# Kernel optimization log

Measured on AMD Instinct MI355X. Metric: run time of the kernel, lower is better.

## Reference

```python
import jax, jax.numpy as jnp
import numpy as np

N = 100000   # nodes
E = 1600000  # edges
IN = 92      # input node feature dim
H = 128      # hidden dim
B = 512      # graphs in batch
GI = 107     # global_info feature dim
L = 5        # conv layers
EPS = 1e-5   # batchnorm eps


def setup_inputs() -> dict:
    key = jax.random.key(0)
    ks = jax.random.split(key, 32)
    s = 0.05
    rn = lambda k, shp: jax.random.normal(k, shp, jnp.float32) * s
    return {
        "x": jax.random.normal(ks[0], (N, IN), jnp.float32),
        "edge_index": jax.random.randint(ks[1], (2, E), 0, N, jnp.int32),
        "edge_dist": jax.random.uniform(ks[2], (E,), jnp.float32),
        "global_info": jax.random.normal(ks[3], (N, GI), jnp.float32),
        "batch": jnp.sort(jax.random.randint(ks[4], (N,), 0, B, jnp.int32)),
        # input projection
        "lin_W": rn(ks[5], (IN, H)), "lin_b": rn(ks[6], (H,)),
        # GCN conv stack
        "conv_W": rn(ks[7], (L, H, H)), "conv_b": rn(ks[8], (L, H)),
        # shared batchnorm affine
        "bn_g": jnp.ones((H,), jnp.float32), "bn_b": jnp.zeros((H,), jnp.float32),
        # global attention
        "gat_in_W": rn(ks[9], (H + GI, H)), "gat_in_b": rn(ks[10], (H,)),
        "gat_lin_W": rn(ks[11], (2, H, H)), "gat_lin_b": rn(ks[12], (2, H)),
        "gat_out_W": rn(ks[13], (H, 1)), "gat_out_b": rn(ks[14], (1,)),
        # Set2Set LSTM (input 2H, hidden H)
        "lstm_Wih": rn(ks[15], (4 * H, 2 * H)), "lstm_Whh": rn(ks[16], (4 * H, H)),
        "lstm_bih": rn(ks[17], (4 * H,)), "lstm_bhh": rn(ks[18], (4 * H,)),
        # MLP head (in_dim = 2H)
        "mlp_W": rn(ks[19], (2 * H, 2 * H)), "mlp_b": rn(ks[20], (2 * H,)),
        "out1_W": rn(ks[21], (2 * H, 32)), "out1_b": rn(ks[22], (32,)),
        "out2_W": rn(ks[23], (32, 1)), "out2_b": rn(ks[24], (1,)),
    }


def _segment_softmax(e, seg, num_seg):
    m = jax.ops.segment_max(e, seg, num_seg)
    ex = jnp.exp(e - m[seg])
    return ex / jax.ops.segment_sum(ex, seg, num_seg)[seg]


def reference(x, edge_index, edge_dist, global_info, batch,
              lin_W, lin_b, conv_W, conv_b, bn_g, bn_b,
              gat_in_W, gat_in_b, gat_lin_W, gat_lin_b, gat_out_W, gat_out_b,
              lstm_Wih, lstm_Whh, lstm_bih, lstm_bhh,
              mlp_W, mlp_b, out1_W, out1_b, out2_W, out2_b):
    src, dst = edge_index[0], edge_index[1]

    x = jax.nn.relu(x @ lin_W + lin_b)

    # GCN normalization (improved=True: self-loop weight 2), identical each layer
    deg = jax.ops.segment_sum(edge_dist, dst, N) + 2.0
    dinv = jax.lax.rsqrt(deg)
    enorm = dinv[src] * edge_dist * dinv[dst]   # [E]
    self_norm = 2.0 * dinv * dinv               # [N]

    prev = x
    for l in range(L):
        xw = x @ conv_W[l]                                                  # [N,H]
        agg = (jax.ops.segment_sum(enorm[:, None] * xw[src], dst, N)
               + self_norm[:, None] * xw + conv_b[l])
        mu = agg.mean(0)
        var = agg.var(0)
        h = bn_g * (agg - mu) * jax.lax.rsqrt(var + EPS) + bn_b             # BN (batch stats)
        x = h + prev                                                         # residual; dropout=identity (eval)
        prev = x

    # global attention -> per-graph softmax node weights
    g = jax.nn.relu(jnp.concatenate([x, global_info], axis=-1) @ gat_in_W + gat_in_b)
    for l in range(2):
        g = jax.nn.relu(g @ gat_lin_W[l] + gat_lin_b[l])
    e = (g @ gat_out_W + gat_out_b)[:, 0]                                    # [N]
    w = _segment_softmax(e, batch, B)
    x = x * w[:, None]

    # Set2Set pooling, 3 processing steps
    hs = jnp.zeros((B, H), x.dtype)
    cs = jnp.zeros((B, H), x.dtype)
    q_star = jnp.zeros((B, 2 * H), x.dtype)
    for _ in range(3):
        gates = q_star @ lstm_Wih.T + hs @ lstm_Whh.T + lstm_bih + lstm_bhh
        i, f, gg, o = jnp.split(gates, 4, axis=-1)
        cs = jax.nn.sigmoid(f) * cs + jax.nn.sigmoid(i) * jnp.tanh(gg)
        hs = jax.nn.sigmoid(o) * jnp.tanh(cs)
        q = hs                                                                # [B,H]
        en = jnp.sum(x * q[batch], axis=-1)                                   # [N]
        a = _segment_softmax(en, batch, B)
        r = jax.ops.segment_sum(a[:, None] * x, batch, B)                      # [B,H]
        q_star = jnp.concatenate([q, r], axis=-1)

    # MLP head
    y = jax.nn.relu(q_star @ mlp_W + mlp_b)
    y = jax.nn.relu(y @ out1_W + out1_b)
    y = y @ out2_W + out2_b
    return y.reshape(1, -1)
```

## Files before the change

### kernel.cpp

```cpp
#include <hip/hip_runtime.h>
#include <math.h>

#define NN 100000
#define NE 1600000
#define DIN 92
#define H 128
#define NB 512
#define DGI 107
#define NL 5

typedef unsigned short u16;
typedef unsigned int u32;
typedef unsigned long long u64;
typedef short bf16x8 __attribute__((ext_vector_type(8)));
typedef float f32x4 __attribute__((ext_vector_type(4)));
typedef _Float16 f16;
typedef _Float16 f16x8 __attribute__((ext_vector_type(8)));
typedef unsigned short u16x8 __attribute__((ext_vector_type(8)));

__device__ __forceinline__ u16 f2bf(float f) {
    unsigned u = __builtin_bit_cast(unsigned, f);
    u += 0x7FFF + ((u >> 16) & 1);
    return (u16)(u >> 16);
}
__device__ __forceinline__ float bf2f(u16 h) {
    unsigned u = ((unsigned)h) << 16;
    return __builtin_bit_cast(float, u);
}

struct WJobs {
    const float* W[9];
    long long eoff[9];
    int K[9];
    int Kpad[9];
};

__global__ void __launch_bounds__(128) k_splitW_all(WJobs jobs, u16* __restrict__ wthi, u16* __restrict__ wtlo)
{
    int j = blockIdx.z;
    int c = blockIdx.x;
    int k = blockIdx.y * 128 + threadIdx.x;
    int Kp = jobs.Kpad[j];
    if (k >= Kp) return;
    const float* W = jobs.W[j];
    float v = (k < jobs.K[j]) ? W[(size_t)k * H + c] : 0.f;
    u16 h = f2bf(v);
    float r = v - bf2f(h);
    size_t o = (size_t)jobs.eoff[j] + (size_t)c * Kp + k;
    wthi[o] = h;
    wtlo[o] = f2bf(r);
}

#define GBM 128

template<int RELU, int OMODE, int KPAD, int AMODE>
__global__ void __launch_bounds__(256) k_mgemm(
    const u16* __restrict__ A1hi, const u16* __restrict__ A1lo, int lda1, int K1,
    const u16* __restrict__ A2hi, const u16* __restrict__ A2lo, int lda2,
    const u16* __restrict__ Wthi, const u16* __restrict__ Wtlo,
    const float* __restrict__ bias,
    float* __restrict__ Cf, u16* __restrict__ Chi, u16* __restrict__ Clo, int ldsp,
    f16* __restrict__ Ch,
    const float* __restrict__ Gow, const float* __restrict__ GobP, float* __restrict__ Esc,
    const f16* __restrict__ Agg, const float* __restrict__ Sc, const float* __restrict__ Sh,
    u16* __restrict__ WBhi, u16* __restrict__ WBlo,
    const float* __restrict__ Fsrc, int FW,
    int M)
{
    __shared__ __align__(16) u16 As[2][128][40];
    __shared__ __align__(16) u16 Ws[2][128][40];
    int tid = threadIdx.x;
    int w = tid >> 6, l = tid & 63;
    int row0 = blockIdx.x * GBM;
    int lr = l & 15, kq = l >> 4;

    f32x4 acc[2][8];
#pragma unroll
    for (int rf = 0; rf < 2; ++rf)
#pragma unroll
        for (int cf = 0; cf < 8; ++cf)
            acc[rf][cf] = (f32x4){0.f, 0.f, 0.f, 0.f};

#pragma unroll
    for (int k0 = 0; k0 < KPAD; k0 += 32) {
        const u16* sAh = (k0 < K1) ? A1hi : A2hi;
        const u16* sAl = (k0 < K1) ? A1lo : A2lo;
        int ldc = (k0 < K1) ? lda1 : lda2;
        int kc = (k0 < K1) ? k0 : (k0 - K1);
#pragma unroll
        for (int i = 0; i < 2; ++i) {
            int chunk = tid + i * 256;
            int r = chunk >> 2, q = chunk & 3;
            int gr = row0 + r; if (gr >= M) gr = M - 1;
            int col0 = kc + q * 8;
            int4 va, vb;
            bool fsplit = (AMODE == 2 && k0 < K1) || (AMODE == 3 && k0 >= K1);
            if (fsplit) {
                u16x8 hh, ll;
#pragma unroll
                for (int j = 0; j < 8; ++j) {
                    int c = col0 + j;
                    float v = (c < FW) ? Fsrc[(size_t)gr * FW + c] : 0.f;
                    u16 h = f2bf(v);
                    hh[j] = h;
                    ll[j] = f2bf(v - bf2f(h));
                }
                va = __builtin_bit_cast(int4, hh);
                vb = __builtin_bit_cast(int4, ll);
            } else {
                va = *(const int4*)(sAh + (size_t)gr * ldc + col0);
                vb = *(const int4*)(sAl + (size_t)gr * ldc + col0);
                if ((AMODE == 1 || AMODE == 3) && k0 < K1) {
                    f16x8 av = *(const f16x8*)(Agg + (size_t)gr * H + col0);
                    u16x8 hh = __builtin_bit_cast(u16x8, va);
                    u16x8 ll = __builtin_bit_cast(u16x8, vb);
                    float4 sc0 = *(const float4*)(Sc + col0);
                    float4 sc1 = *(const float4*)(Sc + col0 + 4);
                    float4 sh0 = *(const float4*)(Sh + col0);
                    float4 sh1 = *(const float4*)(Sh + col0 + 4);
                    float scv[8] = {sc0.x, sc0.y, sc0.z, sc0.w, sc1.x, sc1.y, sc1.z, sc1.w};
                    float shv[8] = {sh0.x, sh0.y, sh0.z, sh0.w, sh1.x, sh1.y, sh1.z, sh1.w};
#pragma unroll
                    for (int j = 0; j < 8; ++j) {
                        float v = bf2f(hh[j]) + bf2f(ll[j]) + (float)av[j] * scv[j] + shv[j];
                        u16 h = f2bf(v);
                        hh[j] = h;
                        ll[j] = f2bf(v - bf2f(h));
                    }
                    va = __builtin_bit_cast(int4, hh);
                    vb = __builtin_bit_cast(int4, ll);
                    *(int4*)(WBhi + (size_t)gr * lda1 + col0) = va;
                    *(int4*)(WBlo + (size_t)gr * lda1 + col0) = vb;
                }
            }
            int4 wa = *(const int4*)(Wthi + (size_t)r * KPAD + k0 + q * 8);
            int4 wb = *(const int4*)(Wtlo + (size_t)r * KPAD + k0 + q * 8);
            *(int4*)&As[0][r][q * 8] = va;
            *(int4*)&As[1][r][q * 8] = vb;
            *(int4*)&Ws[0][r][q * 8] = wa;
            *(int4*)&Ws[1][r][q * 8] = wb;
        }
        __syncthreads();

        bf16x8 aH[2], aL[2];
#pragma unroll
        for (int rf = 0; rf < 2; ++rf) {
            aH[rf] = *(const bf16x8*)&As[0][w * 32 + rf * 16 + lr][kq * 8];
            aL[rf] = *(const bf16x8*)&As[1][w * 32 + rf * 16 + lr][kq * 8];
        }
#pragma unroll
        for (int cf = 0; cf < 8; ++cf) {
            bf16x8 bH = *(const bf16x8*)&Ws[0][cf * 16 + lr][kq * 8];
            bf16x8 bL = *(const bf16x8*)&Ws[1][cf * 16 + lr][kq * 8];
#pragma unroll
            for (int rf = 0; rf < 2; ++rf) {
                acc[rf][cf] = __builtin_amdgcn_mfma_f32_16x16x32_bf16(aH[rf], bH, acc[rf][cf], 0, 0, 0);
                acc[rf][cf] = __builtin_amdgcn_mfma_f32_16x16x32_bf16(aH[rf], bL, acc[rf][cf], 0, 0, 0);
                acc[rf][cf] = __builtin_amdgcn_mfma_f32_16x16x32_bf16(aL[rf], bH, acc[rf][cf], 0, 0, 0);
            }
        }
        __syncthreads();
    }

    if (OMODE == 3) {
        float gowv[8], bvv[8];
#pragma unroll
        for (int cf = 0; cf < 8; ++cf) {
            gowv[cf] = Gow[cf * 16 + lr];
            bvv[cf] = bias[cf * 16 + lr];
        }
        float gob0 = GobP[0];
#pragma unroll
        for (int rf = 0; rf < 2; ++rf) {
#pragma unroll
            for (int r = 0; r < 4; ++r) {
                float part = 0.f;
#pragma unroll
                for (int cf = 0; cf < 8; ++cf) {
                    float v = fmaxf(acc[rf][cf][r] + bvv[cf], 0.f);
                    part += v * gowv[cf];
                }
                part += __shfl_xor(part, 1);
                part += __shfl_xor(part, 2);
                part += __shfl_xor(part, 4);
                part += __shfl_xor(part, 8);
                int grow = row0 + w * 32 + rf * 16 + kq * 4 + r;
                if (lr == 0 && grow < M) Esc[grow] = part + gob0;
            }
        }
        return;
    }

#pragma unroll
    for (int cf = 0; cf < 8; ++cf) {
        int col = cf * 16 + lr;
        float bv = bias ? bias[col] : 0.f;
#pragma unroll
        for (int rf = 0; rf < 2; ++rf) {
#pragma unroll
            for (int r = 0; r < 4; ++r) {
                int grow = row0 + w * 32 + rf * 16 + kq * 4 + r;
                if (grow < M) {
                    float v = acc[rf][cf][r] + bv;
                    if (RELU) v = fmaxf(v, 0.f);
                    if (OMODE == 0) Cf[(size_t)grow * H + col] = v;
                    if (OMODE == 1) {
                        u16 hh = f2bf(v);
                        Chi[(size_t)grow * ldsp + col] = hh;
                        Clo[(size_t)grow * ldsp + col] = f2bf(v - bf2f(hh));
                    }
                    if (OMODE == 2) Ch[(size_t)grow * H + col] = (f16)v;
                }
            }
        }
    }
}

__global__ void __launch_bounds__(256) k_deg2(const int* __restrict__ dst, const float* __restrict__ ed,
                                              u64* __restrict__ degcnt, int* __restrict__ rank)
{
    int e = blockIdx.x * 256 + threadIdx.x;
    if (e < NE) {
        int d = dst[e];
        u64 pk = ((u64)1 << 40) | (u64)(ed[e] * 16777216.0f);
        u64 old = atomicAdd(&degcnt[d], pk);
        rank[e] = (int)(old >> 40);
    }
}

__global__ void __launch_bounds__(256) k_dinv2(const u64* __restrict__ degcnt,
                                               float* __restrict__ dinv, float* __restrict__ selfn,
                                               int* __restrict__ cnt)
{
    int n = blockIdx.x * 256 + threadIdx.x;
    if (n < NN) {
        u64 v = degcnt[n];
        int c = (int)(v >> 40);
        float deg = (float)((double)(v & (((u64)1 << 40) - 1)) * (1.0 / 16777216.0));
        float d = deg + 2.0f;
        float dv = 1.0f / sqrtf(d);
        dinv[n] = dv;
        selfn[n] = 2.0f * dv * dv;
        cnt[n] = c;
    }
}

__global__ void __launch_bounds__(256) k_blocksum(const int* __restrict__ cnt, int* __restrict__ bsum, int n)
{
    __shared__ int red[256];
    int t = threadIdx.x;
    int base = blockIdx.x * 1024;
    int s = 0;
#pragma unroll
    for (int j = 0; j < 4; ++j) {
        int i = base + j * 256 + t;
        if (i < n) s += cnt[i];
    }
    red[t] = s; __syncthreads();
    for (int off = 128; off; off >>= 1) {
        if (t < off) red[t] += red[t + off];
        __syncthreads();
    }
    if (t == 0) bsum[blockIdx.x] = red[0];
}

__global__ void k_scanbsum(const int* __restrict__ bsum, int* __restrict__ boff, int nb,
                           int* __restrict__ rp_last, int total)
{
    if (threadIdx.x == 0 && blockIdx.x == 0) {
        int s = 0;
        for (int i = 0; i < nb; ++i) { boff[i] = s; s += bsum[i]; }
        rp_last[0] = total;
    }
}

__global__ void __launch_bounds__(1024) k_scanchunk(const int* __restrict__ cnt, const int* __restrict__ boff,
                                                    int* __restrict__ rp, int n)
{
    __shared__ int sc[1024];
    int t = threadIdx.x;
    int i = blockIdx.x * 1024 + t;
    int own = (i < n) ? cnt[i] : 0;
    sc[t] = own;
    __syncthreads();
    for (int off = 1; off < 1024; off <<= 1) {
        int v = (t >= off) ? sc[t - off] : 0;
        __syncthreads();
        sc[t] += v;
        __syncthreads();
    }
    if (i < n) rp[i] = boff[blockIdx.x] + sc[t] - own;
}

__global__ void __launch_bounds__(256) k_place2(const int* __restrict__ src, const int* __restrict__ dst,
                                                const float* __restrict__ ed, const float* __restrict__ dinv,
                                                const int* __restrict__ rp, const int* __restrict__ rank,
                                                u32* __restrict__ ew)
{
    int e = blockIdx.x * 256 + threadIdx.x;
    if (e < NE) {
        int d = dst[e], s = src[e];
        int pos = rp[d] + rank[e];
        float w = dinv[s] * ed[e] * dinv[d];
        f16 wh = (f16)w;
        u32 wb = (u32)__builtin_bit_cast(u16, wh);
        ew[pos] = (wb << 17) | (u32)s;
    }
}

__global__ void __launch_bounds__(256) k_spmm(
    const f16* __restrict__ xwh, const int* __restrict__ rp,
    const u32* __restrict__ ew,
    const float* __restrict__ selfn, const float* __restrict__ cb,
    f16* __restrict__ aggh, double* __restrict__ stats)
{
    int tid = threadIdx.x;
    int slot = tid >> 4;
    int sl = tid & 15;
    int f0 = sl * 8;
    float cbv[8], psum[8], psq[8];
#pragma unroll
    for (int j = 0; j < 8; ++j) { cbv[j] = cb[f0 + j]; psum[j] = 0.f; psq[j] = 0.f; }
    int base = blockIdx.x * 32 + slot * 2;

    for (int i = 0; i < 2; ++i) {
        int n = base + i;
        if (n >= NN) break;
        f16x8 xv = *(const f16x8*)(xwh + (size_t)n * H + f0);
        float sn = selfn[n];
        float a0[8], a1[8], a2[8], a3[8];
#pragma unroll
        for (int j = 0; j < 8; ++j) {
            a0[j] = sn * (float)xv[j] + cbv[j];
            a1[j] = 0.f; a2[j] = 0.f; a3[j] = 0.f;
        }
        int e = rp[n], end = rp[n + 1];
        for (; e + 4 <= end; e += 4) {
            u32 p0 = ew[e], p1 = ew[e + 1], p2 = ew[e + 2], p3 = ew[e + 3];
            float w0 = (float)__builtin_bit_cast(f16, (u16)(p0 >> 17));
            float w1 = (float)__builtin_bit_cast(f16, (u16)(p1 >> 17));
            float w2 = (float)__builtin_bit_cast(f16, (u16)(p2 >> 17));
            float w3 = (float)__builtin_bit_cast(f16, (u16)(p3 >> 17));
            f16x8 v0 = *(const f16x8*)(xwh + (size_t)(p0 & 0x1FFFF) * H + f0);
            f16x8 v1 = *(const f16x8*)(xwh + (size_t)(p1 & 0x1FFFF) * H + f0);
            f16x8 v2 = *(const f16x8*)(xwh + (size_t)(p2 & 0x1FFFF) * H + f0);
            f16x8 v3 = *(const f16x8*)(xwh + (size_t)(p3 & 0x1FFFF) * H + f0);
#pragma unroll
            for (int j = 0; j < 8; ++j) {
                a0[j] += w0 * (float)v0[j];
                a1[j] += w1 * (float)v1[j];
                a2[j] += w2 * (float)v2[j];
                a3[j] += w3 * (float)v3[j];
            }
        }
        for (; e < end; ++e) {
            u32 p = ew[e];
            float w0 = (float)__builtin_bit_cast(f16, (u16)(p >> 17));
            f16x8 v0 = *(const f16x8*)(xwh + (size_t)(p & 0x1FFFF) * H + f0);
#pragma unroll
            for (int j = 0; j < 8; ++j) a0[j] += w0 * (float)v0[j];
        }
        float ax[8];
        f16x8 ah;
#pragma unroll
        for (int j = 0; j < 8; ++j) {
            ax[j] = (a0[j] + a1[j]) + (a2[j] + a3[j]);
            psum[j] += ax[j];
            psq[j] += ax[j] * ax[j];
            ah[j] = (f16)ax[j];
        }
        __builtin_nontemporal_store(ah, (f16x8*)(aggh + (size_t)n * H + f0));
    }

    __shared__ float ssum[16][128], ssq[16][128];
#pragma unroll
    for (int j = 0; j < 8; ++j) { ssum[slot][f0 + j] = psum[j]; ssq[slot][f0 + j] = psq[j]; }
    __syncthreads();
    if (tid < 128) {
        float s = 0.f, q = 0.f;
#pragma unroll
        for (int j = 0; j < 16; ++j) { s += ssum[j][tid]; q += ssq[j][tid]; }
        atomicAdd(&stats[tid], (double)s);
        atomicAdd(&stats[128 + tid], (double)q);
    }
}

__global__ void k_finalize(double* __restrict__ stats, const float* __restrict__ bn_g,
                           const float* __restrict__ bn_b, float* __restrict__ scale,
                           float* __restrict__ shift)
{
    int f = threadIdx.x;
    double mu = stats[f] / (double)NN;
    double var = stats[128 + f] / (double)NN - mu * mu;
    double rs = 1.0 / sqrt(var + 1e-5);
    float sc = (float)((double)bn_g[f] * rs);
    scale[f] = sc;
    shift[f] = (float)((double)bn_b[f] - mu * (double)sc);
    stats[f] = 0.0;
    stats[128 + f] = 0.0;
}

__global__ void __launch_bounds__(256) k_goff2(const int* __restrict__ batch, int* __restrict__ goff)
{
    int n = blockIdx.x * 256 + threadIdx.x;
    if (n >= NN) return;
    int b = batch[n];
    if (n == 0) {
        for (int j = 0; j <= b; ++j) goff[j] = 0;
    }
    int nb = (n == NN - 1) ? NB : batch[n + 1];
    for (int j = b + 1; j <= nb; ++j) goff[j] = n + 1;
}

__global__ void __launch_bounds__(256) k_segsoftmax(const float* __restrict__ e, const int* __restrict__ goff,
                                                    float* __restrict__ w)
{
    int b = blockIdx.x;
    int beg = goff[b], end = goff[b + 1];
    int t = threadIdx.x;
    __shared__ float red[8], red2[8];
    float m = -INFINITY;
    for (int i = beg + t; i < end; i += 256) m = fmaxf(m, e[i]);
    for (int off = 32; off; off >>= 1) m = fmaxf(m, __shfl_down(m, off));
    if ((t & 63) == 0) red[t >> 6] = m;
    __syncthreads();
    float m0 = fmaxf(fmaxf(red[0], red[1]), fmaxf(red[2], red[3]));
    float s = 0.f;
    for (int i = beg + t; i < end; i += 256) s += expf(e[i] - m0);
    for (int off = 32; off; off >>= 1) s += __shfl_down(s, off);
    if ((t & 63) == 0) red2[t >> 6] = s;
    __syncthreads();
    float s0 = red2[0] + red2[1] + red2[2] + red2[3];
    for (int i = beg + t; i < end; i += 256) w[i] = expf(e[i] - m0) / s0;
}

__global__ void __launch_bounds__(256) k_scalex16(const u16* __restrict__ xhi, const u16* __restrict__ xlo,
                                                  const float* __restrict__ w, f16* __restrict__ xf)
{
    int i8 = blockIdx.x * 256 + threadIdx.x;
    if (i8 >= NN * 16) return;
    float ww = w[i8 >> 4];
    u16x8 hh = ((const u16x8*)xhi)[i8];
    u16x8 ll = ((const u16x8*)xlo)[i8];
    f16x8 v;
#pragma unroll
    for (int j = 0; j < 8; ++j)
        v[j] = (f16)((bf2f(hh[j]) + bf2f(ll[j])) * ww);
    ((f16x8*)xf)[i8] = v;
}

__device__ __forceinline__ float sigmoidf_(float v) { return 1.f / (1.f + expf(-v)); }

__global__ void __launch_bounds__(256) k_gateslstm(
    const float* __restrict__ qstar, const float* __restrict__ Wih, const float* __restrict__ Whh,
    const float* __restrict__ bih, const float* __restrict__ bhh,
    float* __restrict__ cs, float* __restrict__ hs)
{
    __shared__ float qs[8][256];
    __shared__ float hh[8][128];
    __shared__ float gs[8][512];
    int t = threadIdx.x;
    int b0 = blockIdx.x * 8;
    for (int i = t; i < 8 * 256; i += 256) qs[i >> 8][i & 255] = qstar[b0 * 256 + i];
    for (int i = t; i < 8 * 128; i += 256) hh[i >> 7][i & 127] = hs[b0 * 128 + i];
    __syncthreads();
    for (int gg = t; gg < 512; gg += 256) {
        float acc[8];
        float bb = bih[gg] + bhh[gg];
#pragma unroll
        for (int g = 0; g < 8; ++g) acc[g] = bb;
        const float4* w4 = (const float4*)(Wih + (size_t)gg * 256);
        for (int k = 0; k < 64; ++k) {
            float4 w = w4[k];
#pragma unroll
            for (int g = 0; g < 8; ++g) {
                float4 q = *(const float4*)&qs[g][k * 4];
                acc[g] += q.x * w.x + q.y * w.y + q.z * w.z + q.w * w.w;
            }
        }
        const float4* v4 = (const float4*)(Whh + (size_t)gg * 128);
        for (int k = 0; k < 32; ++k) {
            float4 w = v4[k];
#pragma unroll
            for (int g = 0; g < 8; ++g) {
                float4 q = *(const float4*)&hh[g][k * 4];
                acc[g] += q.x * w.x + q.y * w.y + q.z * w.z + q.w * w.w;
            }
        }
#pragma unroll
        for (int g = 0; g < 8; ++g) gs[g][gg] = acc[g];
    }
    __syncthreads();
    for (int i = t; i < 1024; i += 256) {
        int g = i >> 7, f = i & 127;
        int idx = (b0 + g) * 128 + f;
        float gi = gs[g][f], gf = gs[g][128 + f], gg2 = gs[g][256 + f], go = gs[g][384 + f];
        float c = sigmoidf_(gf) * cs[idx] + sigmoidf_(gi) * tanhf(gg2);
        cs[idx] = c;
        hs[idx] = sigmoidf_(go) * tanhf(c);
    }
}

__global__ void __launch_bounds__(256) k_s2s(const f16* __restrict__ x16, const float* __restrict__ hs,
                                             const int* __restrict__ goff,
                                             float* __restrict__ esc, float* __restrict__ qstar)
{
    __shared__ float q[128];
    __shared__ float red[4], red2[4];
    __shared__ float partr[3][128];
    int b = blockIdx.x, t = threadIdx.x;
    int beg = goff[b], end = goff[b + 1];
    if (t < 128) q[t] = hs[b * 128 + t];
    __syncthreads();

    int wv = t >> 6, ln = t & 63;
    float m = -INFINITY;
    for (int i = beg + wv; i < end; i += 4) {
        u32 xp = *(const u32*)(x16 + (size_t)i * H + ln * 2);
        float xl = (float)__builtin_bit_cast(f16, (u16)(xp & 0xFFFF));
        float xh = (float)__builtin_bit_cast(f16, (u16)(xp >> 16));
        float pd = xl * q[ln * 2] + xh * q[ln * 2 + 1];
        for (int off = 32; off; off >>= 1) pd += __shfl_down(pd, off);
        pd = __shfl(pd, 0);
        if (ln == 0) esc[i] = pd;
        m = fmaxf(m, pd);
    }
    if (ln == 0) red[wv] = m;
    __syncthreads();
    float m0 = fmaxf(fmaxf(red[0], red[1]), fmaxf(red[2], red[3]));
    float s = 0.f;
    for (int i = beg + t; i < end; i += 256) {
        float e = expf(esc[i] - m0);
        esc[i] = e;
        s += e;
    }
    for (int off = 32; off; off >>= 1) s += __shfl_down(s, off);
    if (ln == 0) red2[wv] = s;
    __syncthreads();
    float s0 = red2[0] + red2[1] + red2[2] + red2[3];
    float inv = (s0 > 0.f) ? 1.f / s0 : 0.f;
    int q4 = t >> 6, f2 = (t & 63) * 2;
    float a0 = 0.f, a1 = 0.f;
    for (int i = beg + q4; i < end; i += 4) {
        float w = esc[i];
        u32 xp = *(const u32*)(x16 + (size_t)i * H + f2);
        a0 += w * (float)__builtin_bit_cast(f16, (u16)(xp & 0xFFFF));
        a1 += w * (float)__builtin_bit_cast(f16, (u16)(xp >> 16));
    }
    if (q4 > 0) { partr[q4 - 1][f2] = a0; partr[q4 - 1][f2 + 1] = a1; }
    __syncthreads();
    if (q4 == 0) {
        a0 += partr[0][f2] + partr[1][f2] + partr[2][f2];
        a1 += partr[0][f2 + 1] + partr[1][f2 + 1] + partr[2][f2 + 1];
        qstar[b * 256 + f2] = q[f2];
        qstar[b * 256 + f2 + 1] = q[f2 + 1];
        qstar[b * 256 + 128 + f2] = a0 * inv;
        qstar[b * 256 + 128 + f2 + 1] = a1 * inv;
    }
}

__global__ void __launch_bounds__(256) k_head1(const float* __restrict__ qstar, const float* __restrict__ W,
                                               const float* __restrict__ bias, float* __restrict__ y1)
{
    __shared__ float qs[256];
    int b = blockIdx.x, t = threadIdx.x;
    qs[t] = qstar[b * 256 + t];
    __syncthreads();
    float acc = bias[t];
    for (int k = 0; k < 256; ++k) acc += qs[k] * W[k * 256 + t];
    y1[b * 256 + t] = fmaxf(acc, 0.f);
}

__global__ void __launch_bounds__(256) k_head2(const float* __restrict__ y1, const float* __restrict__ W1,
                                               const float* __restrict__ b1, const float* __restrict__ W2,
                                               const float* __restrict__ b2, float* __restrict__ out)
{
    __shared__ float ys[256];
    __shared__ float z[32];
    int b = blockIdx.x, t = threadIdx.x;
    ys[t] = y1[b * 256 + t];
    __syncthreads();
    if (t < 32) {
        float acc = b1[t];
        for (int k = 0; k < 256; ++k) acc += ys[k] * W1[k * 32 + t];
        z[t] = fmaxf(acc, 0.f);
    }
    __syncthreads();
    if (t == 0) {
        float s = b2[0];
        for (int j = 0; j < 32; ++j) s += z[j] * W2[j];
        out[b] = s;
    }
}

extern "C" void kernel_launch(void* const* d_in, const int* in_sizes, int n_in,
                              void* d_out, int out_size, void* d_ws, size_t ws_size,
                              hipStream_t stream)
{
    const float* in_x        = (const float*)d_in[0];
    const int*   edge_index  = (const int*)d_in[1];
    const float* edge_dist   = (const float*)d_in[2];
    const float* global_info = (const float*)d_in[3];
    const int*   batch       = (const int*)d_in[4];
    const float* lin_W  = (const float*)d_in[5];
    const float* lin_b  = (const float*)d_in[6];
    const float* conv_W = (const float*)d_in[7];
    const float* conv_b = (const float*)d_in[8];
    const float* bn_g   = (const float*)d_in[9];
    const float* bn_b   = (const float*)d_in[10];
    const float* gat_in_W  = (const float*)d_in[11];
    const float* gat_in_b  = (const float*)d_in[12];
    const float* gat_lin_W = (const float*)d_in[13];
    const float* gat_lin_b = (const float*)d_in[14];
    const float* gat_out_W = (const float*)d_in[15];
    const float* gat_out_b = (const float*)d_in[16];
    const float* lstm_Wih = (const float*)d_in[17];
    const float* lstm_Whh = (const float*)d_in[18];
    const float* lstm_bih = (const float*)d_in[19];
    const float* lstm_bhh = (const float*)d_in[20];
    const float* mlp_W  = (const float*)d_in[21];
    const float* mlp_b  = (const float*)d_in[22];
    const float* out1_W = (const float*)d_in[23];
    const float* out1_b = (const float*)d_in[24];
    const float* out2_W = (const float*)d_in[25];
    const float* out2_b = (const float*)d_in[26];
    float* out = (float*)d_out;

    const int* e_src = edge_index;
    const int* e_dst = edge_index + NE;

    char* p = (char*)d_ws;
    auto alloc = [&](size_t bytes) -> void* {
        void* r = (void*)p;
        p += (bytes + 255) & ~(size_t)255;
        return r;
    };
    u16*    cx_hi = (u16*)alloc((size_t)NN * H * 2);
    u16*    cx_lo = (u16*)alloc((size_t)NN * H * 2);
    float*  xw    = (float*)alloc((size_t)NN * H * 4);
    float*  agg   = (float*)alloc((size_t)NN * H * 4);
    u16*    wthi  = (u16*)alloc((size_t)160000 * 2);
    u16*    wtlo  = (u16*)alloc((size_t)160000 * 2);
    float*  dinv  = (float*)alloc((size_t)NN * 4);
    float*  selfn = (float*)alloc((size_t)NN * 4);
    int*    cnt   = (int*)alloc((size_t)NN * 4);
    int*    rp    = (int*)alloc((size_t)(NN + 1) * 4);
    int*    bsum  = (int*)alloc(128 * 4);
    int*    boff  = (int*)alloc(128 * 4);
    u32*    ew    = (u32*)alloc((size_t)NE * 4);
    double* stats = (double*)alloc(256 * 8);
    float*  scale = (float*)alloc(128 * 4);
    float*  shift = (float*)alloc(128 * 4);

    f16*   xwh    = (f16*)xw;
    f16*   aggh   = (f16*)agg;
    u64*   degcnt = (u64*)agg;
    int*   rank   = (int*)((char*)agg + (1 << 20));
    u16*   gi_hi  = (u16*)xw;
    u16*   gi_lo  = gi_hi + (size_t)NN * H;
    float* esc    = dinv;
    float* wn     = selfn;
    int*   goff   = cnt;
    float* hs     = (float*)ew;
    float* csb    = hs + NB * H;
    float* qstar  = csb + NB * H;
    float* y1     = qstar + NB * 2 * H;

    const int GB_E = (NE + 255) / 256;
    const int GB_N = (NN + 255) / 256;
    const int NCH = (NN + 1023) / 1024;
    const int GB_MG = (NN + GBM - 1) / GBM;
    const int GB_SPMM = (NN + 31) / 32;
    const int GB_V8 = (NN * 16) / 256 + 1;

    WJobs jobs;
    const float* Wl[9] = {lin_W, conv_W, conv_W + (size_t)H * H, conv_W + (size_t)2 * H * H,
                          conv_W + (size_t)3 * H * H, conv_W + (size_t)4 * H * H,
                          gat_in_W, gat_lin_W, gat_lin_W + (size_t)H * H};
    int Ks[9]  = {DIN, H, H, H, H, H, H + DGI, H, H};
    int Kps[9] = {96, H, H, H, H, H, 256, H, H};
    long long eoffs[9];
    long long eo = 0;
    for (int i = 0; i < 9; ++i) {
        jobs.W[i] = Wl[i]; jobs.K[i] = Ks[i]; jobs.Kpad[i] = Kps[i]; jobs.eoff[i] = eo;
        eoffs[i] = eo;
        eo += (long long)128 * Kps[i];
    }
    k_splitW_all<<<dim3(128, 2, 9), 128, 0, stream>>>(jobs, wthi, wtlo);

    hipMemsetAsync(degcnt, 0, (size_t)NN * 8, stream);
    hipMemsetAsync(stats, 0, 256 * 8, stream);
    k_deg2<<<GB_E, 256, 0, stream>>>(e_dst, edge_dist, degcnt, rank);
    k_dinv2<<<GB_N, 256, 0, stream>>>(degcnt, dinv, selfn, cnt);
    k_blocksum<<<NCH, 256, 0, stream>>>(cnt, bsum, NN);
    k_scanbsum<<<1, 64, 0, stream>>>(bsum, boff, NCH, rp + NN, NE);
    k_scanchunk<<<NCH, 1024, 0, stream>>>(cnt, boff, rp, NN);
    k_place2<<<GB_E, 256, 0, stream>>>(e_src, e_dst, edge_dist, dinv, rp, rank, ew);

    k_mgemm<1, 1, 96, 2><<<GB_MG, 256, 0, stream>>>(nullptr, nullptr, H, 96, nullptr, nullptr, H,
                                                    wthi + eoffs[0], wtlo + eoffs[0], lin_b,
                                                    nullptr, cx_hi, cx_lo, H, nullptr,
                                                    nullptr, nullptr, nullptr,
                                                    nullptr, nullptr, nullptr, nullptr, nullptr,
                                                    in_x, DIN, NN);

    for (int l = 0; l < NL; ++l) {
        if (l == 0) {
            k_mgemm<0, 2, 128, 0><<<GB_MG, 256, 0, stream>>>(cx_hi, cx_lo, H, H, cx_hi, cx_lo, H,
                                                             wthi + eoffs[1 + l], wtlo + eoffs[1 + l], nullptr,
                                                             nullptr, nullptr, nullptr, 0, xwh,
                                                             nullptr, nullptr, nullptr,
                                                             nullptr, nullptr, nullptr, nullptr, nullptr,
                                                             nullptr, 0, NN);
        } else {
            k_mgemm<0, 2, 128, 1><<<GB_MG, 256, 0, stream>>>(cx_hi, cx_lo, H, H, cx_hi, cx_lo, H,
                                                             wthi + eoffs[1 + l], wtlo + eoffs[1 + l], nullptr,
                                                             nullptr, nullptr, nullptr, 0, xwh,
                                                             nullptr, nullptr, nullptr,
                                                             aggh, scale, shift, cx_hi, cx_lo,
                                                             nullptr, 0, NN);
        }
        k_spmm<<<GB_SPMM, 256, 0, stream>>>(xwh, rp, ew, selfn, conv_b + (size_t)l * H, aggh, stats);
        k_finalize<<<1, 128, 0, stream>>>(stats, bn_g, bn_b, scale, shift);
    }

    k_mgemm<1, 1, 256, 3><<<GB_MG, 256, 0, stream>>>(cx_hi, cx_lo, H, H, nullptr, nullptr, H,
                                                     wthi + eoffs[6], wtlo + eoffs[6], gat_in_b,
                                                     nullptr, gi_hi, gi_lo, H, nullptr,
                                                     nullptr, nullptr, nullptr,
                                                     aggh, scale, shift, cx_hi, cx_lo,
                                                     global_info, DGI, NN);
    k_mgemm<1, 1, 128, 0><<<GB_MG, 256, 0, stream>>>(gi_hi, gi_lo, H, H, gi_hi, gi_lo, H,
                                                     wthi + eoffs[7], wtlo + eoffs[7], gat_lin_b,
                                                     nullptr, gi_hi, gi_lo, H, nullptr,
                                                     nullptr, nullptr, nullptr,
                                                     nullptr, nullptr, nullptr, nullptr, nullptr,
                                                     nullptr, 0, NN);
    k_mgemm<1, 3, 128, 0><<<GB_MG, 256, 0, stream>>>(gi_hi, gi_lo, H, H, gi_hi, gi_lo, H,
                                                     wthi + eoffs[8], wtlo + eoffs[8], gat_lin_b + H,
                                                     nullptr, nullptr, nullptr, 0, nullptr,
                                                     gat_out_W, gat_out_b, esc,
                                                     nullptr, nullptr, nullptr, nullptr, nullptr,
                                                     nullptr, 0, NN);
    k_goff2<<<GB_N, 256, 0, stream>>>(batch, goff);
    k_segsoftmax<<<NB, 256, 0, stream>>>(esc, goff, wn);
    k_scalex16<<<GB_V8, 256, 0, stream>>>(cx_hi, cx_lo, wn, (f16*)xw);

    hipMemsetAsync(hs, 0, (size_t)NB * H * 4, stream);
    hipMemsetAsync(csb, 0, (size_t)NB * H * 4, stream);
    hipMemsetAsync(qstar, 0, (size_t)NB * 2 * H * 4, stream);
    for (int it = 0; it < 3; ++it) {
        k_gateslstm<<<NB / 8, 256, 0, stream>>>(qstar, lstm_Wih, lstm_Whh, lstm_bih, lstm_bhh, csb, hs);
        k_s2s<<<NB, 256, 0, stream>>>((const f16*)xw, hs, goff, esc, qstar);
    }

    k_head1<<<NB, 256, 0, stream>>>(qstar, mlp_W, mlp_b, y1);
    k_head2<<<NB, 256, 0, stream>>>(y1, out1_W, out1_b, out2_W, out2_b, out);
}
```

Measured before the change: 1.379 ms.

## Drop low-precision split for attention-gate activations and fuse softmax with x scaling

The gate MLP's intermediate activations are now stored as bf16 high parts only (new output mode 4). The following GEMMs skip loading the low part and drop the third MFMA term through a new ALO template flag. This removes one global load, one LDS store and one MFMA per fragment in two GEMMs, plus the low-part writes, at the cost of reduced accuracy in the attention logits. Segment softmax and the x-scaling-to-fp16 step are fused into one per-graph kernel that stores the exponentials in place, removing a launch and a pass over the weights.

Measured after the change: 1.357 ms. No clear change (-1.6%).

```diff
diff --git a/kernel.cpp b/kernel.cpp
--- a/kernel.cpp
+++ b/kernel.cpp
@@ -53,7 +53,7 @@
 
 #define GBM 128
 
-template<int RELU, int OMODE, int KPAD, int AMODE>
+template<int RELU, int OMODE, int KPAD, int AMODE, int ALO>
 __global__ void __launch_bounds__(256) k_mgemm(
     const u16* __restrict__ A1hi, const u16* __restrict__ A1lo, int lda1, int K1,
     const u16* __restrict__ A2hi, const u16* __restrict__ A2lo, int lda2,
@@ -94,6 +94,7 @@
             int gr = row0 + r; if (gr >= M) gr = M - 1;
             int col0 = kc + q * 8;
             int4 va, vb;
+            vb = (int4){0, 0, 0, 0};
             bool fsplit = (AMODE == 2 && k0 < K1) || (AMODE == 3 && k0 >= K1);
             if (fsplit) {
                 u16x8 hh, ll;
@@ -109,7 +110,7 @@
                 vb = __builtin_bit_cast(int4, ll);
             } else {
                 va = *(const int4*)(sAh + (size_t)gr * ldc + col0);
-                vb = *(const int4*)(sAl + (size_t)gr * ldc + col0);
+                if (ALO) vb = *(const int4*)(sAl + (size_t)gr * ldc + col0);
                 if ((AMODE == 1 || AMODE == 3) && k0 < K1) {
                     f16x8 av = *(const f16x8*)(Agg + (size_t)gr * H + col0);
                     u16x8 hh = __builtin_bit_cast(u16x8, va);
@@ -136,7 +137,7 @@
             int4 wa = *(const int4*)(Wthi + (size_t)r * KPAD + k0 + q * 8);
             int4 wb = *(const int4*)(Wtlo + (size_t)r * KPAD + k0 + q * 8);
             *(int4*)&As[0][r][q * 8] = va;
-            *(int4*)&As[1][r][q * 8] = vb;
+            if (ALO) *(int4*)&As[1][r][q * 8] = vb;
             *(int4*)&Ws[0][r][q * 8] = wa;
             *(int4*)&Ws[1][r][q * 8] = wb;
         }
@@ -146,7 +147,7 @@
 #pragma unroll
         for (int rf = 0; rf < 2; ++rf) {
             aH[rf] = *(const bf16x8*)&As[0][w * 32 + rf * 16 + lr][kq * 8];
-            aL[rf] = *(const bf16x8*)&As[1][w * 32 + rf * 16 + lr][kq * 8];
+            if (ALO) aL[rf] = *(const bf16x8*)&As[1][w * 32 + rf * 16 + lr][kq * 8];
         }
 #pragma unroll
         for (int cf = 0; cf < 8; ++cf) {
@@ -156,7 +157,8 @@
             for (int rf = 0; rf < 2; ++rf) {
                 acc[rf][cf] = __builtin_amdgcn_mfma_f32_16x16x32_bf16(aH[rf], bH, acc[rf][cf], 0, 0, 0);
                 acc[rf][cf] = __builtin_amdgcn_mfma_f32_16x16x32_bf16(aH[rf], bL, acc[rf][cf], 0, 0, 0);
-                acc[rf][cf] = __builtin_amdgcn_mfma_f32_16x16x32_bf16(aL[rf], bH, acc[rf][cf], 0, 0, 0);
+                if (ALO)
+                    acc[rf][cf] = __builtin_amdgcn_mfma_f32_16x16x32_bf16(aL[rf], bH, acc[rf][cf], 0, 0, 0);
             }
         }
         __syncthreads();
@@ -210,6 +212,7 @@
                         Clo[(size_t)grow * ldsp + col] = f2bf(v - bf2f(hh));
                     }
                     if (OMODE == 2) Ch[(size_t)grow * H + col] = (f16)v;
+                    if (OMODE == 4) Chi[(size_t)grow * ldsp + col] = f2bf(v);
                 }
             }
         }
@@ -412,41 +415,42 @@
     for (int j = b + 1; j <= nb; ++j) goff[j] = n + 1;
 }
 
-__global__ void __launch_bounds__(256) k_segsoftmax(const float* __restrict__ e, const int* __restrict__ goff,
-                                                    float* __restrict__ w)
-{
-    int b = blockIdx.x;
+__global__ void __launch_bounds__(256) k_ssmx(float* __restrict__ esc, const int* __restrict__ goff,
+                                              const u16* __restrict__ xhi, const u16* __restrict__ xlo,
+                                              f16* __restrict__ x16)
+{
+    int b = blockIdx.x, t = threadIdx.x;
     int beg = goff[b], end = goff[b + 1];
-    int t = threadIdx.x;
-    __shared__ float red[8], red2[8];
+    __shared__ float red[4], red2[4];
+    int wv = t >> 6, ln = t & 63;
     float m = -INFINITY;
-    for (int i = beg + t; i < end; i += 256) m = fmaxf(m, e[i]);
+    for (int i = beg + t; i < end; i += 256) m = fmaxf(m, esc[i]);
     for (int off = 32; off; off >>= 1) m = fmaxf(m, __shfl_down(m, off));
-    if ((t & 63) == 0) red[t >> 6] = m;
+    if (ln == 0) red[wv] = m;
     __syncthreads();
     float m0 = fmaxf(fmaxf(red[0], red[1]), fmaxf(red[2], red[3]));
     float s = 0.f;
-    for (int i = beg + t; i < end; i += 256) s += expf(e[i] - m0);
+    for (int i = beg + t; i < end; i += 256) {
+        float e = expf(esc[i] - m0);
+        esc[i] = e;
+        s += e;
+    }
     for (int off = 32; off; off >>= 1) s += __shfl_down(s, off);
-    if ((t & 63) == 0) red2[t >> 6] = s;
+    if (ln == 0) red2[wv] = s;
     __syncthreads();
     float s0 = red2[0] + red2[1] + red2[2] + red2[3];
-    for (int i = beg + t; i < end; i += 256) w[i] = expf(e[i] - m0) / s0;
-}
-
-__global__ void __launch_bounds__(256) k_scalex16(const u16* __restrict__ xhi, const u16* __restrict__ xlo,
-                                                  const float* __restrict__ w, f16* __restrict__ xf)
-{
-    int i8 = blockIdx.x * 256 + threadIdx.x;
-    if (i8 >= NN * 16) return;
-    float ww = w[i8 >> 4];
-    u16x8 hh = ((const u16x8*)xhi)[i8];
-    u16x8 ll = ((const u16x8*)xlo)[i8];
-    f16x8 v;
-#pragma unroll
-    for (int j = 0; j < 8; ++j)
-        v[j] = (f16)((bf2f(hh[j]) + bf2f(ll[j])) * ww);
-    ((f16x8*)xf)[i8] = v;
+    float inv = (s0 > 0.f) ? 1.f / s0 : 0.f;
+    int slot = t >> 4, sl = t & 15, f0 = sl * 8;
+    for (int i = beg + slot; i < end; i += 16) {
+        float w = esc[i] * inv;
+        u16x8 hh = *(const u16x8*)(xhi + (size_t)i * H + f0);
+        u16x8 ll = *(const u16x8*)(xlo + (size_t)i * H + f0);
+        f16x8 v;
+#pragma unroll
+        for (int j = 0; j < 8; ++j)
+            v[j] = (f16)((bf2f(hh[j]) + bf2f(ll[j])) * w);
+        *(f16x8*)(x16 + (size_t)i * H + f0) = v;
+    }
 }
 
 __device__ __forceinline__ float sigmoidf_(float v) { return 1.f / (1.f + expf(-v)); }
@@ -657,9 +661,7 @@
     u64*   degcnt = (u64*)agg;
     int*   rank   = (int*)((char*)agg + (1 << 20));
     u16*   gi_hi  = (u16*)xw;
-    u16*   gi_lo  = gi_hi + (size_t)NN * H;
     float* esc    = dinv;
-    float* wn     = selfn;
     int*   goff   = cnt;
     float* hs     = (float*)ew;
     float* csb    = hs + NB * H;
@@ -671,7 +673,6 @@
     const int NCH = (NN + 1023) / 1024;
     const int GB_MG = (NN + GBM - 1) / GBM;
     const int GB_SPMM = (NN + 31) / 32;
-    const int GB_V8 = (NN * 16) / 256 + 1;
 
     WJobs jobs;
     const float* Wl[9] = {lin_W, conv_W, conv_W + (size_t)H * H, conv_W + (size_t)2 * H * H,
@@ -697,54 +698,53 @@
     k_scanchunk<<<NCH, 1024, 0, stream>>>(cnt, boff, rp, NN);
     k_place2<<<GB_E, 256, 0, stream>>>(e_src, e_dst, edge_dist, dinv, rp, rank, ew);
 
-    k_mgemm<1, 1, 96, 2><<<GB_MG, 256, 0, stream>>>(nullptr, nullptr, H, 96, nullptr, nullptr, H,
-                                                    wthi + eoffs[0], wtlo + eoffs[0], lin_b,
-                                                    nullptr, cx_hi, cx_lo, H, nullptr,
-                                                    nullptr, nullptr, nullptr,
-                                                    nullptr, nullptr, nullptr, nullptr, nullptr,
-                                                    in_x, DIN, NN);
+    k_mgemm<1, 1, 96, 2, 1><<<GB_MG, 256, 0, stream>>>(nullptr, nullptr, H, 96, nullptr, nullptr, H,
+                                                       wthi + eoffs[0], wtlo + eoffs[0], lin_b,
+                                                       nullptr, cx_hi, cx_lo, H, nullptr,
+                                                       nullptr, nullptr, nullptr,
+                                                       nullptr, nullptr, nullptr, nullptr, nullptr,
+                                                       in_x, DIN, NN);
 
     for (int l = 0; l < NL; ++l) {
         if (l == 0) {
-            k_mgemm<0, 2, 128, 0><<<GB_MG, 256, 0, stream>>>(cx_hi, cx_lo, H, H, cx_hi, cx_lo, H,
-                                                             wthi + eoffs[1 + l], wtlo + eoffs[1 + l], nullptr,
-                                                             nullptr, nullptr, nullptr, 0, xwh,
-                                                             nullptr, nullptr, nullptr,
-                                                             nullptr, nullptr, nullptr, nullptr, nullptr,
-                                                             nullptr, 0, NN);
+            k_mgemm<0, 2, 128, 0, 1><<<GB_MG, 256, 0, stream>>>(cx_hi, cx_lo, H, H, cx_hi, cx_lo, H,
+                                                                wthi + eoffs[1 + l], wtlo + eoffs[1 + l], nullptr,
+                                                                nullptr, nullptr, nullptr, 0, xwh,
+                                                                nullptr, nullptr, nullptr,
+                                                                nullptr, nullptr, nullptr, nullptr, nullptr,
+                                                                nullptr, 0, NN);
         } else {
-            k_mgemm<0, 2, 128, 1><<<GB_MG, 256, 0, stream>>>(cx_hi, cx_lo, H, H, cx_hi, cx_lo, H,
-                                                             wthi + eoffs[1 + l], wtlo + eoffs[1 + l], nullptr,
-                                                             nullptr, nullptr, nullptr, 0, xwh,
-                                                             nullptr, nullptr, nullptr,
-                                                             aggh, scale, shift, cx_hi, cx_lo,
-                                                             nullptr, 0, NN);
+            k_mgemm<0, 2, 128, 1, 1><<<GB_MG, 256, 0, stream>>>(cx_hi, cx_lo, H, H, cx_hi, cx_lo, H,
+                                                                wthi + eoffs[1 + l], wtlo + eoffs[1 + l], nullptr,
+                                                                nullptr, nullptr, nullptr, 0, xwh,
+                                                                nullptr, nullptr, nullptr,
+                                                                aggh, scale, shift, cx_hi, cx_lo,
+                                                                nullptr, 0, NN);
         }
         k_spmm<<<GB_SPMM, 256, 0, stream>>>(xwh, rp, ew, selfn, conv_b + (size_t)l * H, aggh, stats);
         k_finalize<<<1, 128, 0, stream>>>(stats, bn_g, bn_b, scale, shift);
     }
 
-    k_mgemm<1, 1, 256, 3><<<GB_MG, 256, 0, stream>>>(cx_hi, cx_lo, H, H, nullptr, nullptr, H,
-                                                     wthi + eoffs[6], wtlo + eoffs[6], gat_in_b,
-                                                     nullptr, gi_hi, gi_lo, H, nullptr,
-                                                     nullptr, nullptr, nullptr,
-                                                     aggh, scale, shift, cx_hi, cx_lo,
-                                                     global_info, DGI, NN);
-    k_mgemm<1, 1, 128, 0><<<GB_MG, 256, 0, stream>>>(gi_hi, gi_lo, H, H, gi_hi, gi_lo, H,
-                                                     wthi + eoffs[7], wtlo + eoffs[7], gat_lin_b,
-                                                     nullptr, gi_hi, gi_lo, H, nullptr,
-                                                     nullptr, nullptr, nullptr,
-                                                     nullptr, nullptr, nullptr, nullptr, nullptr,
-                                                     nullptr, 0, NN);
-    k_mgemm<1, 3, 128, 0><<<GB_MG, 256, 0, stream>>>(gi_hi, gi_lo, H, H, gi_hi, gi_lo, H,
-                                                     wthi + eoffs[8], wtlo + eoffs[8], gat_lin_b + H,
-                                                     nullptr, nullptr, nullptr, 0, nullptr,
-                                                     gat_out_W, gat_out_b, esc,
-                                                     nullptr, nullptr, nullptr, nullptr, nullptr,
-                                                     nullptr, 0, NN);
+    k_mgemm<1, 4, 256, 3, 1><<<GB_MG, 256, 0, stream>>>(cx_hi, cx_lo, H, H, nullptr, nullptr, H,
+                                                        wthi + eoffs[6], wtlo + eoffs[6], gat_in_b,
+                                                        nullptr, gi_hi, nullptr, H, nullptr,
+                                                        nullptr, nullptr, nullptr,
+                                                        aggh, scale, shift, cx_hi, cx_lo,
+                                                        global_info, DGI, NN);
+    k_mgemm<1, 4, 128, 0, 0><<<GB_MG, 256, 0, stream>>>(gi_hi, nullptr, H, H, gi_hi, nullptr, H,
+                                                        wthi + eoffs[7], wtlo + eoffs[7], gat_lin_b,
+                                                        nullptr, gi_hi, nullptr, H, nullptr,
+                                                        nullptr, nullptr, nullptr,
+                                                        nullptr, nullptr, nullptr, nullptr, nullptr,
+                                                        nullptr, 0, NN);
+    k_mgemm<1, 3, 128, 0, 0><<<GB_MG, 256, 0, stream>>>(gi_hi, nullptr, H, H, gi_hi, nullptr, H,
+                                                        wthi + eoffs[8], wtlo + eoffs[8], gat_lin_b + H,
+                                                        nullptr, nullptr, nullptr, 0, nullptr,
+                                                        gat_out_W, gat_out_b, esc,
+                                                        nullptr, nullptr, nullptr, nullptr, nullptr,
+                                                        nullptr, 0, NN);
     k_goff2<<<GB_N, 256, 0, stream>>>(batch, goff);
-    k_segsoftmax<<<NB, 256, 0, stream>>>(esc, goff, wn);
-    k_scalex16<<<GB_V8, 256, 0, stream>>>(cx_hi, cx_lo, wn, (f16*)xw);
+    k_ssmx<<<NB, 256, 0, stream>>>(esc, goff, cx_hi, cx_lo, (f16*)xw);
 
     hipMemsetAsync(hs, 0, (size_t)NB * H * 4, stream);
     hipMemsetAsync(csb, 0, (size_t)NB * H * 4, stream);
```
